# Optimization experiments

Measured on AMD Instinct MI355X. Metric: run time of the kernel, lower is better.

## Reference

```python
import jax, jax.numpy as jnp
import numpy as np

ZMAX = 92          # max atomic number in NLH table
BOHR = 0.52917721  # Bohr radius in Angstrom (au.BOHR)
ENERGY_UNIT = 1.0  # multiplier for 'Ha'
N_ATOMS = 100_000
N_EDGES = 6_400_000
TAB = (ZMAX + 1) ** 2  # 8649


def setup_inputs() -> dict:
    key = jax.random.key(0)
    k1, k2, k3, k4, k5, k6, k7 = jax.random.split(key, 7)
    species = jax.random.randint(k1, (N_ATOMS,), 0, 93, dtype=jnp.int32)
    edge_src = jax.random.randint(k2, (N_EDGES,), 0, N_ATOMS, dtype=jnp.int32)
    edge_dst = jax.random.randint(k3, (N_EDGES,), 0, N_ATOMS, dtype=jnp.int32)
    # distances kept away from zero (division by rijs)
    distances = 0.5 + 4.5 * jax.random.uniform(k4, (N_EDGES,), dtype=jnp.float32)
    switch = jax.random.uniform(k5, (N_EDGES,), dtype=jnp.float32)
    CS = jax.random.uniform(k6, (TAB, 3), dtype=jnp.float32)
    ALPHAS = jax.random.uniform(k7, (TAB, 3), dtype=jnp.float32) + 0.5
    return {"species": species, "edge_src": edge_src, "edge_dst": edge_dst,
            "distances": distances, "switch": switch, "CS": CS, "ALPHAS": ALPHAS}


def reference(species, edge_src, edge_dst, distances, switch, CS, ALPHAS):
    # pair index into (zmax+1)^2 coefficient table
    s12 = species[edge_src] + ZMAX * species[edge_dst]
    cs = CS[s12]          # [E, 3]
    alphas = ALPHAS[s12]  # [E, 3]
    Z = jnp.where(species > 0, species.astype(distances.dtype), 0.0)
    # 3-term exponential screening function
    phi = jnp.sum(cs * jnp.exp(-alphas * distances[:, None]), axis=-1)  # [E]
    ereppair = Z[edge_src] * Z[edge_dst] * phi * switch / distances
    erep_atomic = ENERGY_UNIT * 0.5 * BOHR * jax.ops.segment_sum(
        ereppair, edge_src, num_segments=species.shape[0])
    return erep_atomic
```

## Files before the change

kernel.cpp:

```cpp
#include <hip/hip_runtime.h>
#include <hip/hip_fp16.h>


#define ZMAX_C 92
#define TAB93  93
#define NTAB   (TAB93 * TAB93)
#define HALF_BOHR 0.264588605f
#define NBMAX 64
#define APB 2048
#define APB_LOG 11
#define SPLITS 16
#define TPB  1024
#define NW   (TPB / 64)
#define TPB2 256
#define EPT 8
#define BLK_EDGES (TPB * EPT)
#define SPC_CAP 122880

typedef int            ivec4 __attribute__((ext_vector_type(4)));
typedef float          fvec4 __attribute__((ext_vector_type(4)));

#if __has_builtin(__builtin_amdgcn_rcpf)
#define FAST_RCP(x) __builtin_amdgcn_rcpf(x)
#else
#define FAST_RCP(x) (1.0f / (x))
#endif

__device__ __forceinline__ float half_lo(unsigned u) {
    return __half2float(*reinterpret_cast<const __half*>(&u));
}
__device__ __forceinline__ float half_hi(unsigned u) {
    unsigned s = u >> 16;
    return __half2float(*reinterpret_cast<const __half*>(&s));
}

__global__ __launch_bounds__(TPB2) void p0_prep(
    const float* __restrict__ CS, const float* __restrict__ ALPHAS,
    const int* __restrict__ species,
    uint4* __restrict__ tab16, unsigned char* __restrict__ spc8,
    unsigned* __restrict__ cursor, float* __restrict__ out,
    int n_atoms, int nb)
{
    int i = blockIdx.x * TPB2 + threadIdx.x;
    if (i < NTAB) {
        int sd = i / TAB93;
        int ss = i - TAB93 * sd;
        int ref = ss + ZMAX_C * sd;
        float Z = (ss > 0 && sd > 0) ? (float)(ss * sd) : 0.0f;
        __half h[8];
        h[0] = __float2half_rn(CS[3*ref+0] * Z);
        h[1] = __float2half_rn(CS[3*ref+1] * Z);
        h[2] = __float2half_rn(CS[3*ref+2] * Z);
        h[3] = __float2half_rn(-ALPHAS[3*ref+0]);
        h[4] = __float2half_rn(-ALPHAS[3*ref+1]);
        h[5] = __float2half_rn(-ALPHAS[3*ref+2]);
        h[6] = __half(0.0f); h[7] = __half(0.0f);
        tab16[i] = *reinterpret_cast<uint4*>(h);
    }
    if (i < n_atoms) {
        spc8[i] = (unsigned char)species[i];
        out[i] = 0.0f;
    }
    if (i < nb) cursor[i] = 0u;
}

__global__ __launch_bounds__(TPB) void p1_bin_lds(
    const int* __restrict__ edge_src, const int* __restrict__ edge_dst,
    const float* __restrict__ dist, const float* __restrict__ swt,
    const unsigned char* __restrict__ spc8, const uint4* __restrict__ tab16,
    unsigned* __restrict__ pairs, unsigned* __restrict__ cursor,
    int nb, int cap, int n_edges, int n_atoms, int nchunks)
{
    __shared__ unsigned char spcL[SPC_CAP];
    __shared__ unsigned stage[BLK_EDGES];
    __shared__ unsigned histW[NW][NBMAX];
    __shared__ unsigned hist[NBMAX];
    __shared__ unsigned lbase[NBMAX];
    __shared__ unsigned gbase[NBMAX];

    int tid = threadIdx.x, bid = blockIdx.x;
    const int G = gridDim.x;
    int lane = tid & 63, wave = tid >> 6;

    {
        uint4* dv = (uint4*)spcL;
        const uint4* sv = (const uint4*)spc8;
        int n16 = (n_atoms + 15) >> 4;
        for (int i = tid; i < n16; i += TPB) dv[i] = sv[i];
    }
    __syncthreads();

    for (int c = bid; c < nchunks; c += G) {
        ((unsigned*)histW)[tid] = 0u;
        __syncthreads();

        long long wbase = (long long)c * BLK_EDGES + (long long)wave * (64 * EPT);
        unsigned meta[EPT];
        unsigned short s12r[EPT];

        float rv[EPT], wv[EPT];
        {
            long long eA = wbase + lane * 4;
            long long eB = wbase + 256 + lane * 4;
            bool fullB = (eB + 3 < (long long)n_edges);
            if (fullB) {
                fvec4 r4 = *reinterpret_cast<const fvec4*>(dist + eA);
                fvec4 w4 = *reinterpret_cast<const fvec4*>(swt + eA);
                fvec4 r5 = *reinterpret_cast<const fvec4*>(dist + eB);
                fvec4 w5 = *reinterpret_cast<const fvec4*>(swt + eB);
                #pragma unroll
                for (int k = 0; k < 4; ++k) {
                    rv[k] = r4[k];     wv[k] = w4[k];
                    rv[4 + k] = r5[k]; wv[4 + k] = w5[k];
                }
            } else {
                #pragma unroll
                for (int k = 0; k < 4; ++k) {
                    long long ea = eA + k, eb = eB + k;
                    bool va = (ea < (long long)n_edges), vb = (eb < (long long)n_edges);
                    rv[k] = va ? dist[ea] : 1.f;      wv[k] = va ? swt[ea] : 0.f;
                    rv[4 + k] = vb ? dist[eb] : 1.f;  wv[4 + k] = vb ? swt[eb] : 0.f;
                }
            }
        }
        int srcv[EPT], dstv[EPT];
        #pragma unroll
        for (int j = 0; j < EPT / 4; ++j) {
            long long e0 = wbase + j * 256 + lane * 4;
            if (e0 + 3 < (long long)n_edges) {
                ivec4 s4 = *reinterpret_cast<const ivec4*>(edge_src + e0);
                ivec4 d4 = *reinterpret_cast<const ivec4*>(edge_dst + e0);
                #pragma unroll
                for (int k = 0; k < 4; ++k) { srcv[j*4+k] = s4[k]; dstv[j*4+k] = d4[k]; }
            } else {
                #pragma unroll
                for (int k = 0; k < 4; ++k) {
                    long long e = e0 + k;
                    bool v = (e < (long long)n_edges);
                    srcv[j*4+k] = v ? edge_src[e] : 0;
                    dstv[j*4+k] = v ? edge_dst[e] : 0;
                }
            }
        }
        {
            int ssv[EPT], sdv[EPT];
            #pragma unroll
            for (int i = 0; i < EPT; ++i) ssv[i] = spcL[srcv[i]];
            #pragma unroll
            for (int i = 0; i < EPT; ++i) sdv[i] = spcL[dstv[i]];
            #pragma unroll
            for (int i = 0; i < EPT; ++i)
                s12r[i] = (unsigned short)(ssv[i] + TAB93 * sdv[i]);
        }
        uint4 tv[EPT];
        #pragma unroll
        for (int k = 0; k < EPT; ++k) tv[k] = tab16[s12r[k]];

        #pragma unroll
        for (int j = 0; j < EPT / 4; ++j) {
            long long e0 = wbase + j * 256 + lane * 4;
            #pragma unroll
            for (int k = 0; k < 4; ++k) {
                int idx = j * 4 + k;
                meta[idx] = 0u;
                if (e0 + k < (long long)n_edges) {
                    unsigned b    = (unsigned)srcv[idx] >> APB_LOG;
                    unsigned lsrc = (unsigned)srcv[idx] & (APB - 1);
                    unsigned rank = atomicAdd(&histW[wave][b], 1u);
                    meta[idx] = 0x80000000u | (rank << 17) | (b << 11) | lsrc;
                }
            }
        }
        __syncthreads();
        if (tid < 64) {
            unsigned run = 0;
            #pragma unroll
            for (int w = 0; w < NW; ++w) {
                unsigned t = histW[w][tid];
                histW[w][tid] = run;
                run += t;
            }
            unsigned tot = run;
            if (tid < nb) hist[tid] = tot;
            unsigned v = (tid < nb) ? tot : 0u;
            unsigned x = v;
            #pragma unroll
            for (int off = 1; off < 64; off <<= 1) {
                unsigned y = __shfl_up(x, off);
                if ((tid & 63) >= off) x += y;
            }
            if (tid < nb) {
                lbase[tid] = x - v;
                gbase[tid] = v ? atomicAdd(cursor + tid, v) : 0u;
            }
        }
        __syncthreads();

        #pragma unroll
        for (int idx = 0; idx < EPT; ++idx) {
            unsigned m = meta[idx];
            if (!(m & 0x80000000u)) continue;
            float c0 = half_lo(tv[idx].x), c1 = half_hi(tv[idx].x);
            float c2 = half_lo(tv[idx].y), na0 = half_hi(tv[idx].y);
            float na1 = half_lo(tv[idx].z), na2 = half_hi(tv[idx].z);
            float r = rv[idx];
            float phi = c0 * __expf(na0 * r)
                      + c1 * __expf(na1 * r)
                      + c2 * __expf(na2 * r);
            float val = HALF_BOHR * phi * wv[idx] * FAST_RCP(r);
            unsigned b = (m >> 11) & 63u;
            unsigned pos = lbase[b] + histW[wave][b] + ((m >> 17) & 0x3FFFu);
            unsigned short hb = __half_as_ushort(__float2half_rn(val));
            stage[pos] = ((m & (APB - 1)) << 16) | (unsigned)hb;
        }
        __syncthreads();
        for (int b = wave; b < nb; b += NW) {
            unsigned cnt = hist[b], lb = lbase[b], gb = gbase[b];
            unsigned* dst = pairs + (size_t)b * (size_t)cap + gb;
            for (unsigned i = lane; i < cnt; i += 64)
                if (gb + i < (unsigned)cap) dst[i] = stage[lb + i];
        }
    }
}

#define TPBF 256
#define NWF  4
#define BLKF (TPBF * EPT)
__global__ __launch_bounds__(TPBF) void p1_bin(
    const int* __restrict__ edge_src, const int* __restrict__ edge_dst,
    const float* __restrict__ dist, const float* __restrict__ swt,
    const unsigned char* __restrict__ spc8, const uint4* __restrict__ tab16,
    unsigned* __restrict__ pairs, unsigned* __restrict__ cursor,
    int nb, int cap, int n_edges)
{
    __shared__ unsigned stage[BLKF];
    __shared__ unsigned hist4[NWF][NBMAX];
    __shared__ unsigned hist[NBMAX];
    __shared__ unsigned lbase[NBMAX];
    __shared__ unsigned gbase[NBMAX];

    int tid = threadIdx.x;
    ((unsigned*)hist4)[tid] = 0u;
    __syncthreads();

    int lane = tid & 63, wave = tid >> 6;
    long long wbase = (long long)blockIdx.x * BLKF + (long long)wave * (64 * EPT);

    unsigned meta[EPT];
    unsigned short s12r[EPT];
    {
        int srcv[EPT], dstv[EPT];
        #pragma unroll
        for (int j = 0; j < EPT / 4; ++j) {
            long long e0 = wbase + j * 256 + lane * 4;
            if (e0 + 3 < (long long)n_edges) {
                ivec4 s4 = *reinterpret_cast<const ivec4*>(edge_src + e0);
                ivec4 d4 = *reinterpret_cast<const ivec4*>(edge_dst + e0);
                #pragma unroll
                for (int k = 0; k < 4; ++k) { srcv[j*4+k] = s4[k]; dstv[j*4+k] = d4[k]; }
            } else {
                #pragma unroll
                for (int k = 0; k < 4; ++k) {
                    long long e = e0 + k;
                    bool v = (e < (long long)n_edges);
                    srcv[j*4+k] = v ? edge_src[e] : 0;
                    dstv[j*4+k] = v ? edge_dst[e] : 0;
                }
            }
        }
        int ssv[EPT], sdv[EPT];
        #pragma unroll
        for (int i = 0; i < EPT; ++i) ssv[i] = spc8[srcv[i]];
        #pragma unroll
        for (int i = 0; i < EPT; ++i) sdv[i] = spc8[dstv[i]];
        #pragma unroll
        for (int j = 0; j < EPT / 4; ++j) {
            long long e0 = wbase + j * 256 + lane * 4;
            #pragma unroll
            for (int k = 0; k < 4; ++k) {
                int idx = j * 4 + k;
                s12r[idx] = (unsigned short)(ssv[idx] + TAB93 * sdv[idx]);
                meta[idx] = 0u;
                if (e0 + k < (long long)n_edges) {
                    unsigned b    = (unsigned)srcv[idx] >> APB_LOG;
                    unsigned lsrc = (unsigned)srcv[idx] & (APB - 1);
                    unsigned rank = atomicAdd(&hist4[wave][b], 1u);
                    meta[idx] = 0x80000000u | (rank << 17) | (b << 11) | lsrc;
                }
            }
        }
    }
    __syncthreads();
    if (tid < 64) {
        unsigned run = 0;
        #pragma unroll
        for (int w = 0; w < NWF; ++w) {
            unsigned t = hist4[w][tid];
            hist4[w][tid] = run;
            run += t;
        }
        unsigned tot = run;
        if (tid < nb) hist[tid] = tot;
        unsigned v = (tid < nb) ? tot : 0u;
        unsigned x = v;
        #pragma unroll
        for (int off = 1; off < 64; off <<= 1) {
            unsigned y = __shfl_up(x, off);
            if ((tid & 63) >= off) x += y;
        }
        if (tid < nb) {
            lbase[tid] = x - v;
            gbase[tid] = v ? atomicAdd(cursor + tid, v) : 0u;
        }
    }
    __syncthreads();
    {
        long long eA = wbase + lane * 4;
        long long eB = wbase + 256 + lane * 4;
        float rA[4], wA[4], rB[4], wB[4];
        bool fullB = (eB + 3 < (long long)n_edges);
        if (fullB) {
            fvec4 r4 = *reinterpret_cast<const fvec4*>(dist + eA);
            fvec4 w4 = *reinterpret_cast<const fvec4*>(swt + eA);
            fvec4 r5 = *reinterpret_cast<const fvec4*>(dist + eB);
            fvec4 w5 = *reinterpret_cast<const fvec4*>(swt + eB);
            #pragma unroll
            for (int k = 0; k < 4; ++k) {
                rA[k] = r4[k]; wA[k] = w4[k]; rB[k] = r5[k]; wB[k] = w5[k];
            }
        } else {
            #pragma unroll
            for (int k = 0; k < 4; ++k) {
                long long ea = eA + k, eb = eB + k;
                bool va = (ea < (long long)n_edges), vb = (eb < (long long)n_edges);
                rA[k] = va ? dist[ea] : 1.f;  wA[k] = va ? swt[ea] : 0.f;
                rB[k] = vb ? dist[eb] : 1.f;  wB[k] = vb ? swt[eb] : 0.f;
            }
        }
        uint4 tA[4], tB[4];
        #pragma unroll
        for (int k = 0; k < 4; ++k) tA[k] = tab16[s12r[k]];
        #pragma unroll
        for (int k = 0; k < 4; ++k) tB[k] = tab16[s12r[4 + k]];
        #pragma unroll
        for (int g = 0; g < 2; ++g) {
            const float* r = g ? rB : rA;
            const float* w = g ? wB : wA;
            const uint4* t = g ? tB : tA;
            #pragma unroll
            for (int k = 0; k < 4; ++k) {
                int idx = g * 4 + k;
                unsigned m = meta[idx];
                if (!(m & 0x80000000u)) continue;
                float c0 = half_lo(t[k].x), c1 = half_hi(t[k].x);
                float c2 = half_lo(t[k].y), na0 = half_hi(t[k].y);
                float na1 = half_lo(t[k].z), na2 = half_hi(t[k].z);
                float phi = c0 * __expf(na0 * r[k])
                          + c1 * __expf(na1 * r[k])
                          + c2 * __expf(na2 * r[k]);
                float val = HALF_BOHR * phi * w[k] * FAST_RCP(r[k]);
                unsigned b = (m >> 11) & 63u;
                unsigned pos = lbase[b] + hist4[wave][b] + ((m >> 17) & 0x3FFFu);
                unsigned short hb = __half_as_ushort(__float2half_rn(val));
                stage[pos] = ((m & (APB - 1)) << 16) | (unsigned)hb;
            }
        }
    }
    __syncthreads();
    for (int b = wave; b < nb; b += NWF) {
        unsigned cnt = hist[b], lb = lbase[b], gb = gbase[b];
        unsigned* dst = pairs + (size_t)b * (size_t)cap + gb;
        for (unsigned i = lane; i < cnt; i += 64)
            if (gb + i < (unsigned)cap) dst[i] = stage[lb + i];
    }
}

__global__ __launch_bounds__(TPB2) void p2a_reduce(
    const unsigned* __restrict__ pairs, const unsigned* __restrict__ cursor,
    float* __restrict__ out, int cap, int n_atoms)
{
    int b = blockIdx.x / SPLITS;
    int s = blockIdx.x % SPLITS;
    __shared__ float acc[APB];
    for (int i = threadIdx.x; i < APB; i += TPB2) acc[i] = 0.f;
    __syncthreads();
    unsigned cnt = cursor[b];
    if (cnt > (unsigned)cap) cnt = (unsigned)cap;
    unsigned nq = (cnt + 3u) >> 2;
    unsigned qb = (unsigned)((unsigned long long)nq * s / SPLITS);
    unsigned qe = (unsigned)((unsigned long long)nq * (s + 1) / SPLITS);
    const uint4* p4 = (const uint4*)(pairs + (size_t)b * (size_t)cap);
    for (unsigned q = qb + threadIdx.x; q < qe; q += TPB2) {
        uint4 v = p4[q];
        unsigned base = q << 2;
        if (base + 3u < cnt) {
            unsafeAtomicAdd(&acc[v.x >> 16], __half2float(__ushort_as_half((unsigned short)(v.x & 0xFFFFu))));
            unsafeAtomicAdd(&acc[v.y >> 16], __half2float(__ushort_as_half((unsigned short)(v.y & 0xFFFFu))));
            unsafeAtomicAdd(&acc[v.z >> 16], __half2float(__ushort_as_half((unsigned short)(v.z & 0xFFFFu))));
            unsafeAtomicAdd(&acc[v.w >> 16], __half2float(__ushort_as_half((unsigned short)(v.w & 0xFFFFu))));
        } else {
            unsigned vv[4] = {v.x, v.y, v.z, v.w};
            #pragma unroll
            for (int e = 0; e < 4; ++e)
                if (base + (unsigned)e < cnt)
                    unsafeAtomicAdd(&acc[vv[e] >> 16],
                        __half2float(__ushort_as_half((unsigned short)(vv[e] & 0xFFFFu))));
        }
    }
    __syncthreads();
    int abase = b * APB;
    for (int k = threadIdx.x; k < APB; k += TPB2) {
        int atom = abase + k;
        float vv = acc[k];
        if (atom < n_atoms && vv != 0.0f)
            unsafeAtomicAdd(&out[atom], vv);
    }
}

__global__ __launch_bounds__(TPB2) void erep_edges_direct(
    const int* __restrict__ edge_src, const int* __restrict__ edge_dst,
    const float* __restrict__ dist, const float* __restrict__ swt,
    const int* __restrict__ species, const float* __restrict__ CS,
    const float* __restrict__ ALPHAS, float* __restrict__ out, int n_edges)
{
    int e = blockIdx.x * TPB2 + threadIdx.x;
    if (e >= n_edges) return;
    int ss = species[edge_src[e]], sd = species[edge_dst[e]];
    int prod = ss * sd;
    if (prod == 0) return;
    int s12 = ss + ZMAX_C * sd;
    float r = dist[e];
    float phi = CS[3*s12+0] * __expf(-ALPHAS[3*s12+0] * r)
              + CS[3*s12+1] * __expf(-ALPHAS[3*s12+1] * r)
              + CS[3*s12+2] * __expf(-ALPHAS[3*s12+2] * r);
    atomicAdd(out + edge_src[e],
              HALF_BOHR * (float)prod * phi * swt[e] * FAST_RCP(r));
}

extern "C" void kernel_launch(void* const* d_in, const int* in_sizes, int n_in,
                              void* d_out, int out_size, void* d_ws, size_t ws_size,
                              hipStream_t stream)
{
    const int*   species  = (const int*)  d_in[0];
    const int*   edge_src = (const int*)  d_in[1];
    const int*   edge_dst = (const int*)  d_in[2];
    const float* dist     = (const float*)d_in[3];
    const float* swt      = (const float*)d_in[4];
    const float* CS       = (const float*)d_in[5];
    const float* ALPHAS   = (const float*)d_in[6];
    float* out = (float*)d_out;

    int n_atoms = in_sizes[0];
    int n_edges = in_sizes[1];

    int nb = (n_atoms + APB - 1) / APB;
    long long capll = (long long)n_edges / nb + (long long)n_edges / ((long long)nb * 32) + 256;
    int cap = (int)((capll + 31) & ~31LL);

    size_t pairs_sz = ((size_t)nb * (size_t)cap * 4 + 255) & ~(size_t)255;
    size_t cur_sz   = ((size_t)nb * 4 + 255) & ~(size_t)255;
    size_t tab_sz   = ((size_t)NTAB * 16 + 255) & ~(size_t)255;
    size_t spc_sz   = ((size_t)n_atoms + 255) & ~(size_t)255;
    size_t need = pairs_sz + cur_sz + tab_sz + spc_sz;

    if (nb <= NBMAX && n_edges > 0 && ws_size >= need) {
        char* w = (char*)d_ws;
        unsigned*       pairs   = (unsigned*)w;
        unsigned*       cursor  = (unsigned*)(w + pairs_sz);
        uint4*          tab16   = (uint4*)(w + pairs_sz + cur_sz);
        unsigned char*  spc8    = (unsigned char*)(w + pairs_sz + cur_sz + tab_sz);

        int pmax = n_atoms > NTAB ? n_atoms : NTAB;
        p0_prep<<<(pmax + TPB2 - 1) / TPB2, TPB2, 0, stream>>>(
            CS, ALPHAS, species, tab16, spc8, cursor, out, n_atoms, nb);

        if (n_atoms <= SPC_CAP) {
            int dev = 0, ncu = 256;
            (void)hipGetDevice(&dev);
            (void)hipDeviceGetAttribute(&ncu, hipDeviceAttributeMultiprocessorCount, dev);
            int nchunks = (int)(((long long)n_edges + BLK_EDGES - 1) / BLK_EDGES);
            int G = ncu > 0 ? ncu : 256;
            if (G > nchunks) G = nchunks;
            p1_bin_lds<<<G, TPB, 0, stream>>>(
                edge_src, edge_dst, dist, swt, spc8, tab16,
                pairs, cursor, nb, cap, n_edges, n_atoms, nchunks);
        } else {
            p1_bin<<<(n_edges + BLKF - 1) / BLKF, TPBF, 0, stream>>>(
                edge_src, edge_dst, dist, swt, spc8, tab16,
                pairs, cursor, nb, cap, n_edges);
        }

        p2a_reduce<<<nb * SPLITS, TPB2, 0, stream>>>(pairs, cursor, out, cap, n_atoms);
    } else {
        (void)hipMemsetAsync(d_out, 0, (size_t)out_size * sizeof(float), stream);
        erep_edges_direct<<<(n_edges + TPB2 - 1) / TPB2, TPB2, 0, stream>>>(
            edge_src, edge_dst, dist, swt, species, CS, ALPHAS, out, n_edges);
    }
}
```

Measured before the change: 218.0 us.

## Fuse prep, binning and reduction into one cooperative persistent kernel

Merges the table/species prep, the edge binning pass and the per-bin reduction into a single cooperative kernel that uses grid-wide syncs and atomic work counters for dynamic chunk and slice scheduling. This removes two kernel launches and the gaps between them, and drops the non-LDS binning fallback. In exchange it adds two grid barriers, and the binning chunk shrinks to 4 edges per thread, so there are more atomic-dispatch iterations. The reduction now runs with one block per CU at 1024 threads instead of many 256-thread blocks, which may lower parallelism in that phase.

```diff
diff --git a/kernel.cpp b/kernel.cpp
--- a/kernel.cpp
+++ b/kernel.cpp
@@ -1,5 +1,8 @@
 #include <hip/hip_runtime.h>
 #include <hip/hip_fp16.h>
+#include <hip/hip_cooperative_groups.h>
+
+namespace cg = cooperative_groups;
 
 
 #define ZMAX_C 92
@@ -15,6 +18,8 @@
 #define TPB2 256
 #define EPT 8
 #define BLK_EDGES (TPB * EPT)
+#define FEPT 4
+#define FBLK (TPB * FEPT)
 #define SPC_CAP 122880
 
 typedef int            ivec4 __attribute__((ext_vector_type(4)));
@@ -32,6 +37,217 @@
 __device__ __forceinline__ float half_hi(unsigned u) {
     unsigned s = u >> 16;
     return __half2float(*reinterpret_cast<const __half*>(&s));
+}
+
+__global__ __launch_bounds__(TPB) void fused_v2(
+    const int* __restrict__ edge_src, const int* __restrict__ edge_dst,
+    const float* __restrict__ dist, const float* __restrict__ swt,
+    const int* __restrict__ species, const float* __restrict__ CS,
+    const float* __restrict__ ALPHAS,
+    unsigned* __restrict__ pairs, unsigned* __restrict__ cursor,
+    uint4* __restrict__ tab16, unsigned char* __restrict__ spc8,
+    unsigned* __restrict__ syncw,
+    float* __restrict__ out,
+    int n_atoms, int n_edges, int nb, int cap, int nchunks)
+{
+    cg::grid_group grid = cg::this_grid();
+    const int G = gridDim.x;
+
+    __shared__ unsigned char spcL[SPC_CAP];
+    __shared__ unsigned stage[FBLK];
+    __shared__ unsigned histW[NW][NBMAX];
+    __shared__ unsigned hist[NBMAX];
+    __shared__ unsigned lbase[NBMAX];
+    __shared__ unsigned gbase[NBMAX];
+    __shared__ unsigned bcast;
+
+    int tid = threadIdx.x, bid = blockIdx.x;
+    int gtid = bid * TPB + tid;
+    int lane = tid & 63, wave = tid >> 6;
+
+    if (gtid < NTAB) {
+        int sd = gtid / TAB93;
+        int ss = gtid - TAB93 * sd;
+        int ref = ss + ZMAX_C * sd;
+        float Z = (ss > 0 && sd > 0) ? (float)(ss * sd) : 0.0f;
+        __half h[8];
+        h[0] = __float2half_rn(CS[3*ref+0] * Z);
+        h[1] = __float2half_rn(CS[3*ref+1] * Z);
+        h[2] = __float2half_rn(CS[3*ref+2] * Z);
+        h[3] = __float2half_rn(-ALPHAS[3*ref+0]);
+        h[4] = __float2half_rn(-ALPHAS[3*ref+1]);
+        h[5] = __float2half_rn(-ALPHAS[3*ref+2]);
+        h[6] = __half(0.0f); h[7] = __half(0.0f);
+        tab16[gtid] = *reinterpret_cast<uint4*>(h);
+    }
+    for (int a = gtid; a < n_atoms; a += G * TPB) {
+        spc8[a] = (unsigned char)species[a];
+        out[a] = 0.0f;
+    }
+    if (gtid < nb) cursor[gtid] = 0u;
+    if (gtid < 2) syncw[gtid] = 0u;
+    grid.sync();
+
+    {
+        uint4* dv = (uint4*)spcL;
+        const uint4* sv = (const uint4*)spc8;
+        int n16 = (n_atoms + 15) >> 4;
+        for (int i = tid; i < n16; i += TPB) dv[i] = sv[i];
+    }
+
+    for (;;) {
+        if (tid == 0) bcast = atomicAdd(&syncw[0], 1u);
+        ((unsigned*)histW)[tid] = 0u;
+        __syncthreads();
+        int c = (int)bcast;
+        if (c >= nchunks) break;
+
+        long long wbase = (long long)c * FBLK + (long long)wave * (64 * FEPT);
+        long long e0 = wbase + lane * 4;
+
+        float rv[FEPT], wv[FEPT];
+        int srcv[FEPT], dstv[FEPT];
+        bool full = (e0 + 3 < (long long)n_edges);
+        if (full) {
+            fvec4 r4 = *reinterpret_cast<const fvec4*>(dist + e0);
+            fvec4 w4 = *reinterpret_cast<const fvec4*>(swt + e0);
+            ivec4 s4 = *reinterpret_cast<const ivec4*>(edge_src + e0);
+            ivec4 d4 = *reinterpret_cast<const ivec4*>(edge_dst + e0);
+            #pragma unroll
+            for (int k = 0; k < 4; ++k) {
+                rv[k] = r4[k]; wv[k] = w4[k]; srcv[k] = s4[k]; dstv[k] = d4[k];
+            }
+        } else {
+            #pragma unroll
+            for (int k = 0; k < 4; ++k) {
+                long long e = e0 + k;
+                bool v = (e < (long long)n_edges);
+                rv[k] = v ? dist[e] : 1.f;  wv[k] = v ? swt[e] : 0.f;
+                srcv[k] = v ? edge_src[e] : 0;
+                dstv[k] = v ? edge_dst[e] : 0;
+            }
+        }
+        unsigned short s12r[FEPT];
+        {
+            int ssv[FEPT], sdv[FEPT];
+            #pragma unroll
+            for (int i = 0; i < FEPT; ++i) ssv[i] = spcL[srcv[i]];
+            #pragma unroll
+            for (int i = 0; i < FEPT; ++i) sdv[i] = spcL[dstv[i]];
+            #pragma unroll
+            for (int i = 0; i < FEPT; ++i)
+                s12r[i] = (unsigned short)(ssv[i] + TAB93 * sdv[i]);
+        }
+        uint4 tv[FEPT];
+        #pragma unroll
+        for (int k = 0; k < FEPT; ++k) tv[k] = tab16[s12r[k]];
+
+        unsigned meta[FEPT];
+        #pragma unroll
+        for (int k = 0; k < FEPT; ++k) {
+            meta[k] = 0u;
+            if (e0 + k < (long long)n_edges) {
+                unsigned b    = (unsigned)srcv[k] >> APB_LOG;
+                unsigned lsrc = (unsigned)srcv[k] & (APB - 1);
+                unsigned rank = atomicAdd(&histW[wave][b], 1u);
+                meta[k] = 0x80000000u | (rank << 17) | (b << 11) | lsrc;
+            }
+        }
+        __syncthreads();
+        if (tid < 64) {
+            unsigned run = 0;
+            #pragma unroll
+            for (int w = 0; w < NW; ++w) {
+                unsigned t = histW[w][tid];
+                histW[w][tid] = run;
+                run += t;
+            }
+            unsigned tot = run;
+            if (tid < nb) hist[tid] = tot;
+            unsigned v = (tid < nb) ? tot : 0u;
+            unsigned x = v;
+            #pragma unroll
+            for (int off = 1; off < 64; off <<= 1) {
+                unsigned y = __shfl_up(x, off);
+                if ((tid & 63) >= off) x += y;
+            }
+            if (tid < nb) {
+                lbase[tid] = x - v;
+                gbase[tid] = v ? atomicAdd(cursor + tid, v) : 0u;
+            }
+        }
+        __syncthreads();
+
+        #pragma unroll
+        for (int k = 0; k < FEPT; ++k) {
+            unsigned m = meta[k];
+            if (!(m & 0x80000000u)) continue;
+            float c0 = half_lo(tv[k].x), c1 = half_hi(tv[k].x);
+            float c2 = half_lo(tv[k].y), na0 = half_hi(tv[k].y);
+            float na1 = half_lo(tv[k].z), na2 = half_hi(tv[k].z);
+            float r = rv[k];
+            float phi = c0 * __expf(na0 * r)
+                      + c1 * __expf(na1 * r)
+                      + c2 * __expf(na2 * r);
+            float val = HALF_BOHR * phi * wv[k] * FAST_RCP(r);
+            unsigned b = (m >> 11) & 63u;
+            unsigned pos = lbase[b] + histW[wave][b] + ((m >> 17) & 0x3FFFu);
+            unsigned short hb = __half_as_ushort(__float2half_rn(val));
+            stage[pos] = ((m & (APB - 1)) << 16) | (unsigned)hb;
+        }
+        __syncthreads();
+        for (int b = wave; b < nb; b += NW) {
+            unsigned cnt = hist[b], lb = lbase[b], gb = gbase[b];
+            unsigned* dst = pairs + (size_t)b * (size_t)cap + gb;
+            for (unsigned i = lane; i < cnt; i += 64)
+                if (gb + i < (unsigned)cap) dst[i] = stage[lb + i];
+        }
+    }
+    grid.sync();
+
+    float* acc = (float*)stage;
+    int nslices = nb * SPLITS;
+    for (;;) {
+        if (tid == 0) bcast = atomicAdd(&syncw[1], 1u);
+        __syncthreads();
+        int w = (int)bcast;
+        if (w >= nslices) break;
+        int b = w / SPLITS;
+        int s = w % SPLITS;
+        for (int i = tid; i < APB; i += TPB) acc[i] = 0.f;
+        __syncthreads();
+        unsigned cnt = cursor[b];
+        if (cnt > (unsigned)cap) cnt = (unsigned)cap;
+        unsigned nq = (cnt + 3u) >> 2;
+        unsigned qb = (unsigned)((unsigned long long)nq * s / SPLITS);
+        unsigned qe = (unsigned)((unsigned long long)nq * (s + 1) / SPLITS);
+        const uint4* p4 = (const uint4*)(pairs + (size_t)b * (size_t)cap);
+        for (unsigned q = qb + tid; q < qe; q += TPB) {
+            uint4 v = p4[q];
+            unsigned base = q << 2;
+            if (base + 3u < cnt) {
+                unsafeAtomicAdd(&acc[v.x >> 16], __half2float(__ushort_as_half((unsigned short)(v.x & 0xFFFFu))));
+                unsafeAtomicAdd(&acc[v.y >> 16], __half2float(__ushort_as_half((unsigned short)(v.y & 0xFFFFu))));
+                unsafeAtomicAdd(&acc[v.z >> 16], __half2float(__ushort_as_half((unsigned short)(v.z & 0xFFFFu))));
+                unsafeAtomicAdd(&acc[v.w >> 16], __half2float(__ushort_as_half((unsigned short)(v.w & 0xFFFFu))));
+            } else {
+                unsigned vv[4] = {v.x, v.y, v.z, v.w};
+                #pragma unroll
+                for (int e = 0; e < 4; ++e)
+                    if (base + (unsigned)e < cnt)
+                        unsafeAtomicAdd(&acc[vv[e] >> 16],
+                            __half2float(__ushort_as_half((unsigned short)(vv[e] & 0xFFFFu))));
+            }
+        }
+        __syncthreads();
+        int abase = b * APB;
+        for (int k = tid; k < APB; k += TPB) {
+            int atom = abase + k;
+            float vv = acc[k];
+            if (atom < n_atoms && vv != 0.0f)
+                unsafeAtomicAdd(&out[atom], vv);
+        }
+    }
 }
 
 __global__ __launch_bounds__(TPB2) void p0_prep(
@@ -220,158 +436,6 @@
             for (unsigned i = lane; i < cnt; i += 64)
                 if (gb + i < (unsigned)cap) dst[i] = stage[lb + i];
         }
-    }
-}
-
-#define TPBF 256
-#define NWF  4
-#define BLKF (TPBF * EPT)
-__global__ __launch_bounds__(TPBF) void p1_bin(
-    const int* __restrict__ edge_src, const int* __restrict__ edge_dst,
-    const float* __restrict__ dist, const float* __restrict__ swt,
-    const unsigned char* __restrict__ spc8, const uint4* __restrict__ tab16,
-    unsigned* __restrict__ pairs, unsigned* __restrict__ cursor,
-    int nb, int cap, int n_edges)
-{
-    __shared__ unsigned stage[BLKF];
-    __shared__ unsigned hist4[NWF][NBMAX];
-    __shared__ unsigned hist[NBMAX];
-    __shared__ unsigned lbase[NBMAX];
-    __shared__ unsigned gbase[NBMAX];
-
-    int tid = threadIdx.x;
-    ((unsigned*)hist4)[tid] = 0u;
-    __syncthreads();
-
-    int lane = tid & 63, wave = tid >> 6;
-    long long wbase = (long long)blockIdx.x * BLKF + (long long)wave * (64 * EPT);
-
-    unsigned meta[EPT];
-    unsigned short s12r[EPT];
-    {
-        int srcv[EPT], dstv[EPT];
-        #pragma unroll
-        for (int j = 0; j < EPT / 4; ++j) {
-            long long e0 = wbase + j * 256 + lane * 4;
-            if (e0 + 3 < (long long)n_edges) {
-                ivec4 s4 = *reinterpret_cast<const ivec4*>(edge_src + e0);
-                ivec4 d4 = *reinterpret_cast<const ivec4*>(edge_dst + e0);
-                #pragma unroll
-                for (int k = 0; k < 4; ++k) { srcv[j*4+k] = s4[k]; dstv[j*4+k] = d4[k]; }
-            } else {
-                #pragma unroll
-                for (int k = 0; k < 4; ++k) {
-                    long long e = e0 + k;
-                    bool v = (e < (long long)n_edges);
-                    srcv[j*4+k] = v ? edge_src[e] : 0;
-                    dstv[j*4+k] = v ? edge_dst[e] : 0;
-                }
-            }
-        }
-        int ssv[EPT], sdv[EPT];
-        #pragma unroll
-        for (int i = 0; i < EPT; ++i) ssv[i] = spc8[srcv[i]];
-        #pragma unroll
-        for (int i = 0; i < EPT; ++i) sdv[i] = spc8[dstv[i]];
-        #pragma unroll
-        for (int j = 0; j < EPT / 4; ++j) {
-            long long e0 = wbase + j * 256 + lane * 4;
-            #pragma unroll
-            for (int k = 0; k < 4; ++k) {
-                int idx = j * 4 + k;
-                s12r[idx] = (unsigned short)(ssv[idx] + TAB93 * sdv[idx]);
-                meta[idx] = 0u;
-                if (e0 + k < (long long)n_edges) {
-                    unsigned b    = (unsigned)srcv[idx] >> APB_LOG;
-                    unsigned lsrc = (unsigned)srcv[idx] & (APB - 1);
-                    unsigned rank = atomicAdd(&hist4[wave][b], 1u);
-                    meta[idx] = 0x80000000u | (rank << 17) | (b << 11) | lsrc;
-                }
-            }
-        }
-    }
-    __syncthreads();
-    if (tid < 64) {
-        unsigned run = 0;
-        #pragma unroll
-        for (int w = 0; w < NWF; ++w) {
-            unsigned t = hist4[w][tid];
-            hist4[w][tid] = run;
-            run += t;
-        }
-        unsigned tot = run;
-        if (tid < nb) hist[tid] = tot;
-        unsigned v = (tid < nb) ? tot : 0u;
-        unsigned x = v;
-        #pragma unroll
-        for (int off = 1; off < 64; off <<= 1) {
-            unsigned y = __shfl_up(x, off);
-            if ((tid & 63) >= off) x += y;
-        }
-        if (tid < nb) {
-            lbase[tid] = x - v;
-            gbase[tid] = v ? atomicAdd(cursor + tid, v) : 0u;
-        }
-    }
-    __syncthreads();
-    {
-        long long eA = wbase + lane * 4;
-        long long eB = wbase + 256 + lane * 4;
-        float rA[4], wA[4], rB[4], wB[4];
-        bool fullB = (eB + 3 < (long long)n_edges);
-        if (fullB) {
-            fvec4 r4 = *reinterpret_cast<const fvec4*>(dist + eA);
-            fvec4 w4 = *reinterpret_cast<const fvec4*>(swt + eA);
-            fvec4 r5 = *reinterpret_cast<const fvec4*>(dist + eB);
-            fvec4 w5 = *reinterpret_cast<const fvec4*>(swt + eB);
-            #pragma unroll
-            for (int k = 0; k < 4; ++k) {
-                rA[k] = r4[k]; wA[k] = w4[k]; rB[k] = r5[k]; wB[k] = w5[k];
-            }
-        } else {
-            #pragma unroll
-            for (int k = 0; k < 4; ++k) {
-                long long ea = eA + k, eb = eB + k;
-                bool va = (ea < (long long)n_edges), vb = (eb < (long long)n_edges);
-                rA[k] = va ? dist[ea] : 1.f;  wA[k] = va ? swt[ea] : 0.f;
-                rB[k] = vb ? dist[eb] : 1.f;  wB[k] = vb ? swt[eb] : 0.f;
-            }
-        }
-        uint4 tA[4], tB[4];
-        #pragma unroll
-        for (int k = 0; k < 4; ++k) tA[k] = tab16[s12r[k]];
-        #pragma unroll
-        for (int k = 0; k < 4; ++k) tB[k] = tab16[s12r[4 + k]];
-        #pragma unroll
-        for (int g = 0; g < 2; ++g) {
-            const float* r = g ? rB : rA;
-            const float* w = g ? wB : wA;
-            const uint4* t = g ? tB : tA;
-            #pragma unroll
-            for (int k = 0; k < 4; ++k) {
-                int idx = g * 4 + k;
-                unsigned m = meta[idx];
-                if (!(m & 0x80000000u)) continue;
-                float c0 = half_lo(t[k].x), c1 = half_hi(t[k].x);
-                float c2 = half_lo(t[k].y), na0 = half_hi(t[k].y);
-                float na1 = half_lo(t[k].z), na2 = half_hi(t[k].z);
-                float phi = c0 * __expf(na0 * r[k])
-                          + c1 * __expf(na1 * r[k])
-                          + c2 * __expf(na2 * r[k]);
-                float val = HALF_BOHR * phi * w[k] * FAST_RCP(r[k]);
-                unsigned b = (m >> 11) & 63u;
-                unsigned pos = lbase[b] + hist4[wave][b] + ((m >> 17) & 0x3FFFu);
-                unsigned short hb = __half_as_ushort(__float2half_rn(val));
-                stage[pos] = ((m & (APB - 1)) << 16) | (unsigned)hb;
-            }
-        }
-    }
-    __syncthreads();
-    for (int b = wave; b < nb; b += NWF) {
-        unsigned cnt = hist[b], lb = lbase[b], gb = gbase[b];
-        unsigned* dst = pairs + (size_t)b * (size_t)cap + gb;
-        for (unsigned i = lane; i < cnt; i += 64)
-            if (gb + i < (unsigned)cap) dst[i] = stage[lb + i];
     }
 }
 
@@ -461,7 +525,8 @@
     size_t cur_sz   = ((size_t)nb * 4 + 255) & ~(size_t)255;
     size_t tab_sz   = ((size_t)NTAB * 16 + 255) & ~(size_t)255;
     size_t spc_sz   = ((size_t)n_atoms + 255) & ~(size_t)255;
-    size_t need = pairs_sz + cur_sz + tab_sz + spc_sz;
+    size_t syn_sz   = 256;
+    size_t need = pairs_sz + cur_sz + tab_sz + spc_sz + syn_sz;
 
     if (nb <= NBMAX && n_edges > 0 && ws_size >= need) {
         char* w = (char*)d_ws;
@@ -469,28 +534,53 @@
         unsigned*       cursor  = (unsigned*)(w + pairs_sz);
         uint4*          tab16   = (uint4*)(w + pairs_sz + cur_sz);
         unsigned char*  spc8    = (unsigned char*)(w + pairs_sz + cur_sz + tab_sz);
-
-        int pmax = n_atoms > NTAB ? n_atoms : NTAB;
-        p0_prep<<<(pmax + TPB2 - 1) / TPB2, TPB2, 0, stream>>>(
-            CS, ALPHAS, species, tab16, spc8, cursor, out, n_atoms, nb);
-
-        if (n_atoms <= SPC_CAP) {
-            int dev = 0, ncu = 256;
-            (void)hipGetDevice(&dev);
-            (void)hipDeviceGetAttribute(&ncu, hipDeviceAttributeMultiprocessorCount, dev);
-            int nchunks = (int)(((long long)n_edges + BLK_EDGES - 1) / BLK_EDGES);
-            int G = ncu > 0 ? ncu : 256;
-            if (G > nchunks) G = nchunks;
-            p1_bin_lds<<<G, TPB, 0, stream>>>(
-                edge_src, edge_dst, dist, swt, spc8, tab16,
-                pairs, cursor, nb, cap, n_edges, n_atoms, nchunks);
-        } else {
-            p1_bin<<<(n_edges + BLKF - 1) / BLKF, TPBF, 0, stream>>>(
-                edge_src, edge_dst, dist, swt, spc8, tab16,
-                pairs, cursor, nb, cap, n_edges);
-        }
-
-        p2a_reduce<<<nb * SPLITS, TPB2, 0, stream>>>(pairs, cursor, out, cap, n_atoms);
+        unsigned*       syncw   = (unsigned*)(w + pairs_sz + cur_sz + tab_sz + spc_sz);
+
+        int dev = 0, ncu = 256, coop = 0;
+        (void)hipGetDevice(&dev);
+        (void)hipDeviceGetAttribute(&ncu, hipDeviceAttributeMultiprocessorCount, dev);
+        (void)hipDeviceGetAttribute(&coop, hipDeviceAttributeCooperativeLaunch, dev);
+
+        bool launched = false;
+        if (coop && n_atoms <= SPC_CAP) {
+            int occ = 0;
+            (void)hipOccupancyMaxActiveBlocksPerMultiprocessor(&occ, (const void*)fused_v2, TPB, 0);
+            if (occ >= 1 && ncu > 0) {
+                int nchunks = (int)(((long long)n_edges + FBLK - 1) / FBLK);
+                int G = ncu;
+                if (G > nchunks) G = nchunks;
+                if (G < 1) G = 1;
+                void* kargs[] = {
+                    (void*)&edge_src, (void*)&edge_dst, (void*)&dist, (void*)&swt,
+                    (void*)&species, (void*)&CS, (void*)&ALPHAS,
+                    (void*)&pairs, (void*)&cursor, (void*)&tab16, (void*)&spc8,
+                    (void*)&syncw, (void*)&out,
+                    (void*)&n_atoms, (void*)&n_edges, (void*)&nb, (void*)&cap,
+                    (void*)&nchunks };
+                hipError_t err = hipLaunchCooperativeKernel((const void*)fused_v2,
+                                     dim3(G), dim3(TPB), kargs, 0, stream);
+                launched = (err == hipSuccess);
+            }
+        }
+
+        if (!launched) {
+            int pmax = n_atoms > NTAB ? n_atoms : NTAB;
+            p0_prep<<<(pmax + TPB2 - 1) / TPB2, TPB2, 0, stream>>>(
+                CS, ALPHAS, species, tab16, spc8, cursor, out, n_atoms, nb);
+            if (n_atoms <= SPC_CAP) {
+                int nchunks = (int)(((long long)n_edges + BLK_EDGES - 1) / BLK_EDGES);
+                int G = ncu > 0 ? ncu : 256;
+                if (G > nchunks) G = nchunks;
+                p1_bin_lds<<<G, TPB, 0, stream>>>(
+                    edge_src, edge_dst, dist, swt, spc8, tab16,
+                    pairs, cursor, nb, cap, n_edges, n_atoms, nchunks);
+                p2a_reduce<<<nb * SPLITS, TPB2, 0, stream>>>(pairs, cursor, out, cap, n_atoms);
+            } else {
+                (void)hipMemsetAsync(d_out, 0, (size_t)out_size * sizeof(float), stream);
+                erep_edges_direct<<<(n_edges + TPB2 - 1) / TPB2, TPB2, 0, stream>>>(
+                    edge_src, edge_dst, dist, swt, species, CS, ALPHAS, out, n_edges);
+            }
+        }
     } else {
         (void)hipMemsetAsync(d_out, 0, (size_t)out_size * sizeof(float), stream);
         erep_edges_direct<<<(n_edges + TPB2 - 1) / TPB2, TPB2, 0, stream>>>(
```

After: 293.2 us. +34.5%, slower.
